# Performance work log

Measured on AMD Instinct MI355X. Metric: run time of the kernel, lower is better.

Reference implementation:

```python
import jax, jax.numpy as jnp
import numpy as np

N = 96        # num_nodes
D = 64        # emb_size / n_hid
BS = 16
T = 13
G = 1         # num_graph

# all N^2 ordered pairs, receiver-major: edge e=i*N+j has receiver i, sender j
_REC = jnp.repeat(jnp.arange(N), N)
_SEND = jnp.tile(jnp.arange(N), N)


def _lin(shape, key, scale=0.05):
    return (jax.random.normal(key, shape, dtype=jnp.float32) * scale)


def setup_inputs() -> dict:
    key = jax.random.key(0)
    ks = jax.random.split(key, 24)
    inp = {
        "skill_seq": jax.random.randint(ks[0], (BS, T), 0, N, dtype=jnp.int32),
        "adj": jax.random.uniform(ks[1], (G, BS, N, N), dtype=jnp.float32),
        "node_embeddings": jax.random.normal(ks[2], (G, N, D), dtype=jnp.float32),
        # edge MLP
        "W_msg1": _lin((2 * D, D), ks[3]), "b_msg1": jnp.zeros((D,), jnp.float32),
        "W_msg2": _lin((D, D), ks[4]),     "b_msg2": jnp.zeros((D,), jnp.float32),
        # GRU hidden projections (no bias)
        "W_hr": _lin((D, D), ks[5]), "W_hi": _lin((D, D), ks[6]), "W_hh": _lin((D, D), ks[7]),
        # GRU input projections (bias)
        "W_ir": _lin((D, D), ks[8]),  "b_ir": jnp.zeros((D,), jnp.float32),
        "W_ii": _lin((D, D), ks[9]),  "b_ii": jnp.zeros((D,), jnp.float32),
        "W_in": _lin((D, D), ks[10]), "b_in": jnp.zeros((D,), jnp.float32),
        # output MLP
        "W_o1": _lin((D, D), ks[11]), "b_o1": jnp.zeros((D,), jnp.float32),
        "W_o2": _lin((D, D), ks[12]), "b_o2": jnp.zeros((D,), jnp.float32),
        "W_o3": _lin((D, D), ks[13]), "b_o3": jnp.zeros((D,), jnp.float32),
    }
    return inp


def _forward(skill_seq, adj, node_embeddings,
             W_msg1, b_msg1, W_msg2, b_msg2,
             W_hr, W_hi, W_hh,
             W_ir, b_ir, W_ii, b_ii, W_in, b_in,
             W_o1, b_o1, W_o2, b_o2, W_o3, b_o3):
    bs, time_steps = skill_seq.shape
    hidden0 = jnp.zeros((G, bs, N, D), dtype=adj.dtype)
    emb = node_embeddings[0]  # [N, D] (num_graph=1)

    def step(hidden, skill_t):
        # gather senders/receivers over the node axis -> [G, bs, N^2, 2D]
        senders = hidden[:, :, _SEND, :]
        receivers = hidden[:, :, _REC, :]
        pre_msg = jnp.concatenate([senders, receivers], axis=-1)
        msg = jnp.tanh(pre_msg @ W_msg1 + b_msg1)        # [G, bs, N^2, D]
        msg = jnp.tanh(msg @ W_msg2 + b_msg2)
        msg = msg.reshape(G, bs, N, N, D)                # receiver i, sender j
        # mask by adjacency and scatter-sum over senders, then /N
        agg = jnp.einsum('gbij,gbijd->gbid', adj, msg) / N   # [G, bs, N, D]
        inputs = emb[skill_t][None, :, None, :]          # [1, bs, 1, D]
        r = jax.nn.sigmoid(inputs @ W_ir + b_ir + agg @ W_hr)
        i = jax.nn.sigmoid(inputs @ W_ii + b_ii + agg @ W_hi)
        n = jnp.tanh(inputs @ W_in + b_in + r * (agg @ W_hh))
        hidden = (1.0 - i) * n + i * hidden
        pred = jax.nn.relu(hidden @ W_o1 + b_o1)
        pred = jax.nn.relu(pred @ W_o2 + b_o2)
        pred = pred @ W_o3 + b_o3                        # [G, bs, N, D]
        return hidden, pred

    skills_t = skill_seq[:, :time_steps - 1].T           # [T-1, bs]
    _, preds = jax.lax.scan(step, hidden0, skills_t)     # [T-1, G, bs, N, D]
    # torch: stack(dim=1) -> [G, T-1, bs, N, D]; transpose(1,2) -> [G, bs, T-1, N, D]
    return jnp.transpose(preds, (1, 2, 0, 3, 4))


def reference(skill_seq, adj, node_embeddings,
              W_msg1, b_msg1, W_msg2, b_msg2,
              W_hr, W_hi, W_hh,
              W_ir, b_ir, W_ii, b_ii, W_in, b_in,
              W_o1, b_o1, W_o2, b_o2, W_o3, b_o3):
    return _forward(skill_seq, adj, node_embeddings,
                    W_msg1, b_msg1, W_msg2, b_msg2,
                    W_hr, W_hi, W_hh,
                    W_ir, b_ir, W_ii, b_ii, W_in, b_in,
                    W_o1, b_o1, W_o2, b_o2, W_o3, b_o3)
```

## Files before the change

### kernel.cpp

```cpp
#include <hip/hip_runtime.h>

typedef unsigned short ushort_t;
typedef __attribute__((ext_vector_type(8))) short short8;
typedef __attribute__((ext_vector_type(8))) __bf16 bf16x8;
typedef __attribute__((ext_vector_type(4))) float floatx4;

#define NN 96
#define DD 64
#define BSZ 16
#define TSTEP 12
#define JSPLIT 4
#define JPW 24
#define ITILES 6

#define OFF_HALL  0u
#define OFF_E     5111808u
#define OFF_S0    5185536u
#define OFF_S1    5578752u
#define OFF_R0    5971968u
#define OFF_R1    6365184u
#define OFF_PART  6758400u
#define OFF_WSWZ  9904128u
#define OFF_CNT   9977856u
#define HSLOT     98304

union fragU  { short8 s; bf16x8 b; };
union packU  { floatx4 f; unsigned long long u[2]; };

static __device__ __forceinline__ short f2bf(float f){
    union { float f; unsigned u; } v; v.f = f;
    unsigned u = v.u;
    u += 0x7fffu + ((u >> 16) & 1u);
    return (short)(u >> 16);
}
static __device__ __forceinline__ float fast_tanh(float x){
    float p = __expf(2.f * x);
    return (p - 1.f) * __builtin_amdgcn_rcpf(p + 1.f);
}
static __device__ __forceinline__ float fast_sigmoid(float x){
    float p = __expf(-x);
    return __builtin_amdgcn_rcpf(1.f + p);
}
static __device__ __forceinline__ void zero4(floatx4* a){
    floatx4 z = {0.f,0.f,0.f,0.f};
    a[0]=z; a[1]=z; a[2]=z; a[3]=z;
}
static __device__ __forceinline__ floatx4 aload4(const float* p){
    const unsigned long long* s = (const unsigned long long*)p;
    packU pk;
    pk.u[0] = __hip_atomic_load(s,     __ATOMIC_RELAXED, __HIP_MEMORY_SCOPE_AGENT);
    pk.u[1] = __hip_atomic_load(s + 1, __ATOMIC_RELAXED, __HIP_MEMORY_SCOPE_AGENT);
    return pk.f;
}
static __device__ __forceinline__ void astore4(float* p, floatx4 v){
    unsigned long long* d = (unsigned long long*)p;
    packU pk; pk.f = v;
    __hip_atomic_store(d,     pk.u[0], __ATOMIC_RELAXED, __HIP_MEMORY_SCOPE_AGENT);
    __hip_atomic_store(d + 1, pk.u[1], __ATOMIC_RELAXED, __HIP_MEMORY_SCOPE_AGENT);
}
static __device__ __forceinline__ void buildA(const float* sM, int col, int quad, short8& a0, short8& a1){
    floatx4 f0 = *(const floatx4*)&sM[col*68 + quad*8];
    floatx4 f1 = *(const floatx4*)&sM[col*68 + quad*8 + 4];
    floatx4 f2 = *(const floatx4*)&sM[col*68 + 32 + quad*8];
    floatx4 f3 = *(const floatx4*)&sM[col*68 + 32 + quad*8 + 4];
    fragU u0, u1;
    #pragma unroll
    for (int jj = 0; jj < 4; jj++){
        u0.b[jj]   = (__bf16)f0[jj];
        u0.b[4+jj] = (__bf16)f1[jj];
        u1.b[jj]   = (__bf16)f2[jj];
        u1.b[4+jj] = (__bf16)f3[jj];
    }
    a0 = u0.s; a1 = u1.s;
}
static __device__ __forceinline__ void mm16(short8 a0, short8 a1, const short8* wzm, int l, floatx4* acc){
    #pragma unroll
    for (int nt = 0; nt < 4; nt++){
        short8 b0 = wzm[nt*64 + l];
        short8 b1 = wzm[(4 + nt)*64 + l];
        acc[nt] = __builtin_amdgcn_mfma_f32_16x16x32_bf16(a0, b0, acc[nt], 0, 0, 0);
        acc[nt] = __builtin_amdgcn_mfma_f32_16x16x32_bf16(a1, b1, acc[nt], 0, 0, 0);
    }
}
static __device__ __forceinline__ void mm16r(short8 a0, short8 a1, const short8* f, floatx4* acc){
    #pragma unroll
    for (int nt = 0; nt < 4; nt++){
        acc[nt] = __builtin_amdgcn_mfma_f32_16x16x32_bf16(a0, f[nt],     acc[nt], 0, 0, 0);
        acc[nt] = __builtin_amdgcn_mfma_f32_16x16x32_bf16(a1, f[4 + nt], acc[nt], 0, 0, 0);
    }
}
static __device__ __forceinline__ short8 fragB(const float* W, int l, int kc, int nt, int koff){
    short8 r;
    int kbase = koff + kc*32 + ((l >> 4) << 3);
    int n = nt*16 + (l & 15);
    #pragma unroll
    for (int jj = 0; jj < 8; jj++) r[jj] = f2bf(W[(kbase + jj)*64 + n]);
    return r;
}
static __device__ __forceinline__ void mm16g(short8 a0, short8 a1, const float* W, int koff, int l, floatx4* acc){
    #pragma unroll
    for (int nt = 0; nt < 4; nt++){
        short8 b0 = fragB(W, l, 0, nt, koff);
        short8 b1 = fragB(W, l, 1, nt, koff);
        acc[nt] = __builtin_amdgcn_mfma_f32_16x16x32_bf16(a0, b0, acc[nt], 0, 0, 0);
        acc[nt] = __builtin_amdgcn_mfma_f32_16x16x32_bf16(a1, b1, acc[nt], 0, 0, 0);
    }
}

__global__ __launch_bounds__(256) void k_init(
    const float* __restrict__ emb, const float* __restrict__ Wmsg1,
    const float* __restrict__ Wmsg2,
    const float* __restrict__ Whr, const float* __restrict__ Whi, const float* __restrict__ Whh,
    const float* __restrict__ Wir, const float* __restrict__ bir,
    const float* __restrict__ Wii, const float* __restrict__ bii,
    const float* __restrict__ Win, const float* __restrict__ bin,
    const float* __restrict__ Wo1, const float* __restrict__ Wo2, const float* __restrict__ Wo3,
    const float* __restrict__ adj, const float* __restrict__ b1in, const float* __restrict__ b2in,
    const int* __restrict__ skills,
    int* __restrict__ cnt, float* __restrict__ Ef, ushort_t* __restrict__ wswz,
    float* __restrict__ hall, float* __restrict__ S1, float* __restrict__ R1)
{
    __shared__ float sM[16*68];
    __shared__ float sG[3][16*68];
    __shared__ float sE[3*64];
    __shared__ float sRS[16*17];

    int wg = blockIdx.x, tid = threadIdx.x;
    if (wg < 72) {
        int flat = wg*256 + tid;
        int m = flat / 6144; int r = flat % 6144; int s = r >> 6; int d = r & 63;
        const float* W = (m==0)? Wir : (m==1)? Wii : Win;
        const float* B = (m==0)? bir : (m==1)? bii : bin;
        float acc = B[d];
        #pragma unroll 8
        for (int k = 0; k < 64; k++)
            acc += emb[s*64 + k] * W[k*64 + d];
        Ef[flat] = acc;
        if (wg < 5) {
            int c = wg*256 + tid;
            if (c < TSTEP*BSZ*ITILES) cnt[c] = 0;
        }
        return;
    }
    if (wg < 216) {
        int flat = (wg - 72)*256 + tid;
        int m = flat >> 12; int q = flat & 4095;
        int jj = q & 7, lane = (q >> 3) & 63, nt = (q >> 9) & 3, kc = q >> 11;
        int k = kc*32 + ((lane >> 4) << 3) + jj;
        int n = nt*16 + (lane & 15);
        const float* src; int idx = k*64 + n;
        switch (m) {
          case 0: src = Wmsg2; break;
          case 1: src = Whr;  break;
          case 2: src = Whi;  break;
          case 3: src = Whh;  break;
          case 4: src = Wmsg1; break;
          case 5: src = Wmsg1; idx = (64 + k)*64 + n; break;
          case 6: src = Wo1; break;
          case 7: src = Wo2; break;
          default: src = Wo3; break;
        }
        wswz[flat] = (ushort_t)f2bf(src[idx]);
        return;
    }

    int tile = wg - 216; int b = tile / 6, it = tile % 6;
    int w = tid >> 6; int l = tid & 63;
    int quad = l >> 4, col = l & 15;

    {
        int i = tid >> 4, seg = tid & 15;
        const float* arow = &adj[(b*NN + it*16 + i)*NN + seg*6];
        float s = 0.f;
        #pragma unroll
        for (int j = 0; j < 6; j++) s += arow[j];
        sRS[i*17 + seg] = s;
    }
    if (tid < 192) {
        int m = tid >> 6, d = tid & 63;
        int s = skills[b*13 + 0];
        const float* W = (m==0)? Wir : (m==1)? Wii : Win;
        const float* B = (m==0)? bir : (m==1)? bii : bin;
        float acc = B[d];
        #pragma unroll 8
        for (int k = 0; k < 64; k++)
            acc += emb[s*64 + k] * W[k*64 + d];
        sE[tid] = acc;
    }
    __syncthreads();
    if (tid < 16) {
        float s = 0.f;
        #pragma unroll
        for (int q = 0; q < 16; q++) s += sRS[tid*17 + q];
        sRS[tid*17 + 16] = s * (1.f/96.f);
    }
    __syncthreads();

    if (w == 0) {
        float b2v[4];
        #pragma unroll
        for (int nt = 0; nt < 4; nt++) b2v[nt] = b2in[nt*16 + col];
        fragU u0, u1;
        #pragma unroll
        for (int e = 0; e < 8; e++) {
            u0.b[e] = (__bf16)fast_tanh(b1in[quad*8 + e]);
            u1.b[e] = (__bf16)fast_tanh(b1in[32 + quad*8 + e]);
        }
        floatx4 acc[4];
        zero4(acc);
        mm16g(u0.s, u1.s, Wmsg2, 0, l, acc);
        #pragma unroll
        for (int nt = 0; nt < 4; nt++)
          #pragma unroll
          for (int r = 0; r < 4; r++) {
            float m = fast_tanh(acc[nt][r] + b2v[nt]);
            sM[(quad*4 + r)*68 + nt*16 + col] = sRS[(quad*4 + r)*17 + 16] * m;
          }
    }
    __syncthreads();

    if (w < 3) {
        const float* Wg = (w==0)? Whr : (w==1)? Whi : Whh;
        short8 a0, a1;
        buildA(sM, col, quad, a0, a1);
        floatx4 acc[4];
        zero4(acc);
        mm16g(a0, a1, Wg, 0, l, acc);
        #pragma unroll
        for (int nt = 0; nt < 4; nt++)
          #pragma unroll
          for (int r = 0; r < 4; r++)
            sG[w][(quad*4 + r)*68 + nt*16 + col] = acc[nt][r];
    }
    __syncthreads();

    {
        int i = tid >> 4, k4 = (tid & 15)*4;
        float h[4];
        #pragma unroll
        for (int e = 0; e < 4; e++) {
            int d = k4 + e;
            float gi = fast_sigmoid(sE[64 + d] + sG[1][i*68 + d]);
            float gr = fast_sigmoid(sE[d]      + sG[0][i*68 + d]);
            float nv = fast_tanh  (sE[128 + d] + gr * sG[2][i*68 + d]);
            h[e] = (1.f - gi)*nv;
        }
        #pragma unroll
        for (int e = 0; e < 4; e++) sM[i*68 + k4 + e] = h[e];
        floatx4 hv = { h[0], h[1], h[2], h[3] };
        *(floatx4*)&hall[(size_t)1*HSLOT + (b*NN + it*16 + i)*64 + k4] = hv;
    }
    __syncthreads();

    if (w < 2) {
        short8 a0, a1;
        buildA(sM, col, quad, a0, a1);
        floatx4 acc[4];
        zero4(acc);
        mm16g(a0, a1, Wmsg1, w*64, l, acc);
        float* dst = (w == 0) ? S1 : R1;
        #pragma unroll
        for (int nt = 0; nt < 4; nt++)
          #pragma unroll
          for (int r = 0; r < 4; r++)
            dst[(b*NN + it*16 + quad*4 + r)*64 + nt*16 + col] = acc[nt][r];
    }
}

__global__ __launch_bounds__(512, 2) void k_step(
    const float* __restrict__ adj, const float* __restrict__ b1in, const float* __restrict__ b2in,
    const float* __restrict__ Sread, const float* __restrict__ Rread,
    const ushort_t* __restrict__ wswz, float* __restrict__ partial,
    const int* __restrict__ skills, const float* __restrict__ Ef,
    const float* __restrict__ hprev, float* __restrict__ hcur,
    float* __restrict__ Swrite, float* __restrict__ Rwrite,
    int* __restrict__ cnt, int t)
{
    __shared__ float lds[11712];
    __shared__ int sLast;
    float* sS   = lds;
    float* sRB  = lds + 1536;
    float* sAdj = lds + 2624;
    float* sAgg = lds + 3008;

    int wg = blockIdx.x;
    int js = wg / 96; int rem = wg % 96; int b = rem / 6; int it = rem % 6;
    int tid = threadIdx.x; int w = tid >> 6; int l = tid & 63;
    int quad = l >> 4, col = l & 15;
    int j0 = js * JPW;
    floatx4 myp;

    for (int q = tid; q < JPW*16; q += 512) {
        int row = q >> 4, c4 = (q & 15) * 4;
        *(floatx4*)&sS[row*64 + c4] = *(const floatx4*)&Sread[(b*NN + j0 + row)*64 + c4];
    }
    if (tid < 256) {
        int row = tid >> 4, c4 = (tid & 15) * 4;
        floatx4 r4 = *(const floatx4*)&Rread[(b*NN + it*16 + row)*64 + c4];
        floatx4 b4 = *(const floatx4*)&b1in[c4];
        floatx4 o = r4 + b4;
        *(floatx4*)&sRB[row*68 + c4] = o;
    }
    if (tid < 16*JPW) {
        int i = tid / JPW, j = tid % JPW;
        sAdj[tid] = adj[(b*NN + it*16 + i)*NN + j0 + j];
    }
    const short8* wz = (const short8*)wswz;
    short8 w2f[2][4];
    #pragma unroll
    for (int kc = 0; kc < 2; kc++)
      #pragma unroll
      for (int nt = 0; nt < 4; nt++)
        w2f[kc][nt] = wz[(kc*4 + nt)*64 + l];
    float b2v[4];
    #pragma unroll
    for (int nt = 0; nt < 4; nt++) b2v[nt] = b2in[nt*16 + col];
    __syncthreads();

    float rbv[16];
    #pragma unroll
    for (int c = 0; c < 4; c++)
        *(floatx4*)&rbv[c*4] = *(const floatx4*)&sRB[col*68 + (c>>1)*32 + quad*8 + (c&1)*4];

    float agg[4][4];
    #pragma unroll
    for (int nt=0;nt<4;nt++)
      #pragma unroll
      for (int r=0;r<4;r++) agg[nt][r] = 0.f;

    #pragma unroll
    for (int c = 0; c < 3; c++) {
        int jl = w*3 + c;
        float sv[16];
        #pragma unroll
        for (int cc = 0; cc < 4; cc++)
            *(floatx4*)&sv[cc*4] = *(const floatx4*)&sS[jl*64 + (cc>>1)*32 + quad*8 + (cc&1)*4];
        fragU u0, u1;
        #pragma unroll
        for (int e = 0; e < 8; e++) {
            u0.b[e] = (__bf16)fast_tanh(sv[e]   + rbv[e]);
            u1.b[e] = (__bf16)fast_tanh(sv[8+e] + rbv[8+e]);
        }
        floatx4 acc[4];
        zero4(acc);
        #pragma unroll
        for (int nt = 0; nt < 4; nt++) {
            acc[nt] = __builtin_amdgcn_mfma_f32_16x16x32_bf16(u0.s, w2f[0][nt], acc[nt], 0,0,0);
            acc[nt] = __builtin_amdgcn_mfma_f32_16x16x32_bf16(u1.s, w2f[1][nt], acc[nt], 0,0,0);
        }
        float adjv[4];
        #pragma unroll
        for (int r = 0; r < 4; r++) adjv[r] = sAdj[(quad*4 + r)*JPW + jl];
        #pragma unroll
        for (int nt = 0; nt < 4; nt++)
          #pragma unroll
          for (int r = 0; r < 4; r++)
            agg[nt][r] += adjv[r] * fast_tanh(acc[nt][r] + b2v[nt]);
    }
    #pragma unroll
    for (int nt = 0; nt < 4; nt++)
      #pragma unroll
      for (int r = 0; r < 4; r++)
        sAgg[w*1088 + (quad*4 + r)*68 + nt*16 + col] = agg[nt][r];
    __syncthreads();
    if (tid < 256) {
        int i = tid >> 4, k4 = (tid & 15) * 4;
        floatx4 o = {0.f,0.f,0.f,0.f};
        #pragma unroll
        for (int s8 = 0; s8 < 8; s8++)
            o += *(const floatx4*)&sAgg[s8*1088 + i*68 + k4];
        o = o * (1.f/96.f);
        myp = o;
        float* dstp = &partial[((js*BSZ + b)*NN + it*16 + i)*64 + k4];
        if (t == TSTEP - 1) *(floatx4*)dstp = o;
        else                astore4(dstp, o);
    }
    if (t == TSTEP - 1) return;

    __syncthreads();
    if (tid == 0) {
        int old = atomicAdd(&cnt[t*(BSZ*ITILES) + b*ITILES + it], 1);
        sLast = (old == JSPLIT - 1);
    }
    __syncthreads();
    if (!sLast) return;

    float* sM = lds;
    float* sG = lds + 1088;
    float* sH = lds + 4352;
    float* sE = lds + 5376;

    const short8* wzb = (const short8*)wswz;
    short8 fG[8], fSR[8];
    if (w < 3) {
        #pragma unroll
        for (int q = 0; q < 8; q++) fG[q] = wzb[(1 + w)*512 + q*64 + l];
    }
    if (w < 2) {
        #pragma unroll
        for (int q = 0; q < 8; q++) fSR[q] = wzb[(4 + w)*512 + q*64 + l];
    }

    if (tid < 256) {
        int i = tid >> 4, k4 = (tid & 15) * 4;
        floatx4 a = {0.f,0.f,0.f,0.f};
        #pragma unroll
        for (int p = 0; p < JSPLIT; p++) {
            if (p == js) a += myp;
            else         a += aload4(&partial[((p*BSZ + b)*NN + it*16 + i)*64 + k4]);
        }
        *(floatx4*)&sM[i*68 + k4] = a;
        *(floatx4*)&sH[i*64 + k4] = *(const floatx4*)&hprev[(b*NN + it*16 + i)*64 + k4];
    } else if (tid < 448) {
        int q = tid - 256;
        int s = skills[b*13 + t];
        sE[q] = Ef[(q >> 6)*6144 + s*64 + (q & 63)];
    }
    __syncthreads();

    if (w < 3) {
        short8 a0, a1;
        buildA(sM, col, quad, a0, a1);
        floatx4 acc[4];
        zero4(acc);
        mm16r(a0, a1, fG, acc);
        #pragma unroll
        for (int nt = 0; nt < 4; nt++)
          #pragma unroll
          for (int r = 0; r < 4; r++)
            sG[w*1088 + (quad*4 + r)*68 + nt*16 + col] = acc[nt][r];
    }
    __syncthreads();

    if (tid < 256) {
        int i = tid >> 4, k4 = (tid & 15) * 4;
        float h[4];
        #pragma unroll
        for (int e = 0; e < 4; e++) {
            int d = k4 + e;
            float gr = fast_sigmoid(sE[d]       + sG[0*1088 + i*68 + d]);
            float gi = fast_sigmoid(sE[64 + d]  + sG[1*1088 + i*68 + d]);
            float nv = fast_tanh  (sE[128 + d] + gr * sG[2*1088 + i*68 + d]);
            h[e] = (1.f - gi)*nv + gi*sH[i*64 + d];
        }
        #pragma unroll
        for (int e = 0; e < 4; e++) sM[i*68 + k4 + e] = h[e];
        floatx4 hv = { h[0], h[1], h[2], h[3] };
        *(floatx4*)&hcur[(b*NN + it*16 + i)*64 + k4] = hv;
    }
    __syncthreads();

    if (w < 2) {
        short8 a0, a1;
        buildA(sM, col, quad, a0, a1);
        floatx4 acc[4];
        zero4(acc);
        mm16r(a0, a1, fSR, acc);
        float* dst = (w == 0) ? Swrite : Rwrite;
        #pragma unroll
        for (int nt = 0; nt < 4; nt++)
          #pragma unroll
          for (int r = 0; r < 4; r++)
            dst[(b*NN + it*16 + quad*4 + r)*64 + nt*16 + col] = acc[nt][r];
    }
}

__global__ __launch_bounds__(256) void k_out(
    const int* __restrict__ skills, const float* __restrict__ partial,
    const float* __restrict__ Ef, const float* __restrict__ hall,
    const ushort_t* __restrict__ wswz,
    const float* __restrict__ bo1, const float* __restrict__ bo2, const float* __restrict__ bo3,
    float* __restrict__ out)
{
    __shared__ float sT[4][16*68];
    int tid = threadIdx.x; int w = tid >> 6; int l = tid & 63;
    int quad = l >> 4, col = l & 15;
    int g = blockIdx.x*4 + w;
    int ts = g / 96; int rem = g % 96; int b = rem / 6, it = rem % 6;
    float* sm = sT[w];

    if (ts < 11) {
        const float* hsrc = hall + (size_t)(ts + 1)*HSLOT + (b*NN + it*16)*64;
        int i = l >> 2, c0 = (l & 3)*16;
        #pragma unroll
        for (int cc = 0; cc < 4; cc++)
            *(floatx4*)&sm[i*68 + c0 + cc*4] = *(const floatx4*)&hsrc[i*64 + c0 + cc*4];
    } else {
        int i = l >> 2, c0 = (l & 3)*16;
        floatx4 a[4]; zero4(a);
        for (int p = 0; p < JSPLIT; p++) {
            const float* base = &partial[((p*BSZ + b)*NN + it*16 + i)*64 + c0];
            #pragma unroll
            for (int cc = 0; cc < 4; cc++) a[cc] += *(const floatx4*)&base[cc*4];
        }
        #pragma unroll
        for (int cc = 0; cc < 4; cc++) *(floatx4*)&sm[i*68 + c0 + cc*4] = a[cc];

        short8 a0, a1; buildA(sm, col, quad, a0, a1);
        floatx4 Ar[4], Ai[4], Ah[4];
        zero4(Ar); zero4(Ai); zero4(Ah);
        mm16(a0, a1, (const short8*)wswz + 1*512, l, Ar);
        mm16(a0, a1, (const short8*)wswz + 2*512, l, Ai);
        mm16(a0, a1, (const short8*)wswz + 3*512, l, Ah);
        int s = skills[b*13 + 11];
        const float* hp = hall + 11*(size_t)HSLOT;
        #pragma unroll
        for (int nt = 0; nt < 4; nt++) {
            int d = nt*16 + col;
            float er = Ef[0*6144 + s*64 + d];
            float ei = Ef[1*6144 + s*64 + d];
            float en = Ef[2*6144 + s*64 + d];
            #pragma unroll
            for (int r = 0; r < 4; r++) {
                int row = it*16 + quad*4 + r;
                float gr = fast_sigmoid(er + Ar[nt][r]);
                float gi = fast_sigmoid(ei + Ai[nt][r]);
                float nv = fast_tanh  (en + gr*Ah[nt][r]);
                sm[(quad*4 + r)*68 + d] = (1.f - gi)*nv + gi*hp[(b*NN + row)*64 + d];
            }
        }
    }

    float bv1[4], bv2[4], bv3[4];
    #pragma unroll
    for (int nt = 0; nt < 4; nt++) {
        bv1[nt] = bo1[nt*16 + col];
        bv2[nt] = bo2[nt*16 + col];
        bv3[nt] = bo3[nt*16 + col];
    }
    short8 a0, a1;
    floatx4 acc[4];

    buildA(sm, col, quad, a0, a1);
    zero4(acc);
    mm16(a0, a1, (const short8*)wswz + 6*512, l, acc);
    #pragma unroll
    for (int nt = 0; nt < 4; nt++)
      #pragma unroll
      for (int r = 0; r < 4; r++)
        sm[(quad*4 + r)*68 + nt*16 + col] = fmaxf(0.f, acc[nt][r] + bv1[nt]);

    buildA(sm, col, quad, a0, a1);
    zero4(acc);
    mm16(a0, a1, (const short8*)wswz + 7*512, l, acc);
    #pragma unroll
    for (int nt = 0; nt < 4; nt++)
      #pragma unroll
      for (int r = 0; r < 4; r++)
        sm[(quad*4 + r)*68 + nt*16 + col] = fmaxf(0.f, acc[nt][r] + bv2[nt]);

    buildA(sm, col, quad, a0, a1);
    zero4(acc);
    mm16(a0, a1, (const short8*)wswz + 8*512, l, acc);
    #pragma unroll
    for (int nt = 0; nt < 4; nt++)
      #pragma unroll
      for (int r = 0; r < 4; r++)
        out[((b*TSTEP + ts)*NN + it*16 + quad*4 + r)*64 + nt*16 + col] = acc[nt][r] + bv3[nt];
}

extern "C" void kernel_launch(void* const* d_in, const int* in_sizes, int n_in,
                              void* d_out, int out_size, void* d_ws, size_t ws_size,
                              hipStream_t stream) {
    const int*   skills = (const int*)d_in[0];
    const float* adj    = (const float*)d_in[1];
    const float* emb    = (const float*)d_in[2];
    const float* Wmsg1  = (const float*)d_in[3];
    const float* b1     = (const float*)d_in[4];
    const float* Wmsg2  = (const float*)d_in[5];
    const float* b2     = (const float*)d_in[6];
    const float* Whr    = (const float*)d_in[7];
    const float* Whi    = (const float*)d_in[8];
    const float* Whh    = (const float*)d_in[9];
    const float* Wir    = (const float*)d_in[10];
    const float* bir    = (const float*)d_in[11];
    const float* Wii    = (const float*)d_in[12];
    const float* bii    = (const float*)d_in[13];
    const float* Win    = (const float*)d_in[14];
    const float* bin    = (const float*)d_in[15];
    const float* Wo1    = (const float*)d_in[16];
    const float* bo1    = (const float*)d_in[17];
    const float* Wo2    = (const float*)d_in[18];
    const float* bo2    = (const float*)d_in[19];
    const float* Wo3    = (const float*)d_in[20];
    const float* bo3    = (const float*)d_in[21];

    char* ws = (char*)d_ws;
    float*    hall    = (float*)(ws + OFF_HALL);
    float*    Ef      = (float*)(ws + OFF_E);
    float*    S0      = (float*)(ws + OFF_S0);
    float*    S1      = (float*)(ws + OFF_S1);
    float*    R0      = (float*)(ws + OFF_R0);
    float*    R1      = (float*)(ws + OFF_R1);
    float*    partial = (float*)(ws + OFF_PART);
    ushort_t* wswz    = (ushort_t*)(ws + OFF_WSWZ);
    int*      cnt     = (int*)(ws + OFF_CNT);
    float*    out     = (float*)d_out;

    k_init<<<dim3(312), dim3(256), 0, stream>>>(emb, Wmsg1, Wmsg2, Whr, Whi, Whh,
        Wir, bir, Wii, bii, Win, bin, Wo1, Wo2, Wo3,
        adj, b1, b2, skills, cnt, Ef, wswz, hall, S1, R1);

    for (int t = 1; t < TSTEP; t++) {
        const float* Sr = (t & 1) ? S1 : S0;
        const float* Rr = (t & 1) ? R1 : R0;
        float*       Sw = (t & 1) ? S0 : S1;
        float*       Rw = (t & 1) ? R0 : R1;
        k_step<<<dim3(JSPLIT*BSZ*ITILES), dim3(512), 0, stream>>>(
            adj, b1, b2, Sr, Rr, wswz, partial, skills, Ef,
            hall + (size_t)t*HSLOT, hall + (size_t)(t+1)*HSLOT,
            Sw, Rw, cnt, t);
    }
    k_out<<<dim3(288), dim3(256), 0, stream>>>(skills, partial, Ef, hall, wswz,
        bo1, bo2, bo3, out);
}
```

Before: 253.6 us.

## Fold output MLP for earlier timesteps into idle step blocks

Moves the output MLP for timestep t-1 into k_step, where the first non-last block of each tile computes it from the previous hidden state instead of returning idle. The final k_out launch now only handles the last two timesteps, so it shrinks from 288 to 48 blocks. The intent is to hide output-MLP work inside the step kernels' idle blocks and cut the serial tail of k_out. In exchange, k_step carries more code and register pressure, and the tile whose first-arriving block does this work may finish a little later.

```diff
diff --git a/kernel.cpp b/kernel.cpp
--- a/kernel.cpp
+++ b/kernel.cpp
@@ -105,6 +105,48 @@
         acc[nt] = __builtin_amdgcn_mfma_f32_16x16x32_bf16(a0, b0, acc[nt], 0, 0, 0);
         acc[nt] = __builtin_amdgcn_mfma_f32_16x16x32_bf16(a1, b1, acc[nt], 0, 0, 0);
     }
+}
+static __device__ __forceinline__ void mlp_tile(
+    float* sm, const ushort_t* wswz,
+    const float* bo1, const float* bo2, const float* bo3,
+    float* out, int b, int ts, int it, int l, int quad, int col)
+{
+    float bv1[4], bv2[4], bv3[4];
+    #pragma unroll
+    for (int nt = 0; nt < 4; nt++) {
+        bv1[nt] = bo1[nt*16 + col];
+        bv2[nt] = bo2[nt*16 + col];
+        bv3[nt] = bo3[nt*16 + col];
+    }
+    short8 a0, a1;
+    floatx4 acc[4];
+
+    buildA(sm, col, quad, a0, a1);
+    zero4(acc);
+    mm16(a0, a1, (const short8*)wswz + 6*512, l, acc);
+    #pragma unroll
+    for (int nt = 0; nt < 4; nt++)
+      #pragma unroll
+      for (int r = 0; r < 4; r++)
+        sm[(quad*4 + r)*68 + nt*16 + col] = fmaxf(0.f, acc[nt][r] + bv1[nt]);
+
+    buildA(sm, col, quad, a0, a1);
+    zero4(acc);
+    mm16(a0, a1, (const short8*)wswz + 7*512, l, acc);
+    #pragma unroll
+    for (int nt = 0; nt < 4; nt++)
+      #pragma unroll
+      for (int r = 0; r < 4; r++)
+        sm[(quad*4 + r)*68 + nt*16 + col] = fmaxf(0.f, acc[nt][r] + bv2[nt]);
+
+    buildA(sm, col, quad, a0, a1);
+    zero4(acc);
+    mm16(a0, a1, (const short8*)wswz + 8*512, l, acc);
+    #pragma unroll
+    for (int nt = 0; nt < 4; nt++)
+      #pragma unroll
+      for (int r = 0; r < 4; r++)
+        out[((b*TSTEP + ts)*NN + it*16 + quad*4 + r)*64 + nt*16 + col] = acc[nt][r] + bv3[nt];
 }
 
 __global__ __launch_bounds__(256) void k_init(
@@ -274,10 +316,12 @@
     const int* __restrict__ skills, const float* __restrict__ Ef,
     const float* __restrict__ hprev, float* __restrict__ hcur,
     float* __restrict__ Swrite, float* __restrict__ Rwrite,
-    int* __restrict__ cnt, int t)
+    int* __restrict__ cnt,
+    const float* __restrict__ bo1, const float* __restrict__ bo2, const float* __restrict__ bo3,
+    float* __restrict__ out, int t)
 {
     __shared__ float lds[11712];
-    __shared__ int sLast;
+    __shared__ int sLast, sFirst;
     float* sS   = lds;
     float* sRB  = lds + 1536;
     float* sAdj = lds + 2624;
@@ -380,10 +424,22 @@
     __syncthreads();
     if (tid == 0) {
         int old = atomicAdd(&cnt[t*(BSZ*ITILES) + b*ITILES + it], 1);
-        sLast = (old == JSPLIT - 1);
-    }
-    __syncthreads();
-    if (!sLast) return;
+        sLast  = (old == JSPLIT - 1);
+        sFirst = (old == 0);
+    }
+    __syncthreads();
+    if (!sLast) {
+        if (sFirst && w == 0) {
+            float* sm = lds;
+            const float* hsrc = hcur - HSLOT + (b*NN + it*16)*64;
+            int i2 = l >> 2, c0 = (l & 3)*16;
+            #pragma unroll
+            for (int cc = 0; cc < 4; cc++)
+                *(floatx4*)&sm[i2*68 + c0 + cc*4] = *(const floatx4*)&hsrc[i2*64 + c0 + cc*4];
+            mlp_tile(sm, wswz, bo1, bo2, bo3, out, b, t - 1, it, l, quad, col);
+        }
+        return;
+    }
 
     float* sM = lds;
     float* sG = lds + 1088;
@@ -476,11 +532,11 @@
     int tid = threadIdx.x; int w = tid >> 6; int l = tid & 63;
     int quad = l >> 4, col = l & 15;
     int g = blockIdx.x*4 + w;
-    int ts = g / 96; int rem = g % 96; int b = rem / 6, it = rem % 6;
+    int ts = 10 + g / 96; int rem = g % 96; int b = rem / 6, it = rem % 6;
     float* sm = sT[w];
 
-    if (ts < 11) {
-        const float* hsrc = hall + (size_t)(ts + 1)*HSLOT + (b*NN + it*16)*64;
+    if (ts == 10) {
+        const float* hsrc = hall + (size_t)11*HSLOT + (b*NN + it*16)*64;
         int i = l >> 2, c0 = (l & 3)*16;
         #pragma unroll
         for (int cc = 0; cc < 4; cc++)
@@ -520,43 +576,7 @@
             }
         }
     }
-
-    float bv1[4], bv2[4], bv3[4];
-    #pragma unroll
-    for (int nt = 0; nt < 4; nt++) {
-        bv1[nt] = bo1[nt*16 + col];
-        bv2[nt] = bo2[nt*16 + col];
-        bv3[nt] = bo3[nt*16 + col];
-    }
-    short8 a0, a1;
-    floatx4 acc[4];
-
-    buildA(sm, col, quad, a0, a1);
-    zero4(acc);
-    mm16(a0, a1, (const short8*)wswz + 6*512, l, acc);
-    #pragma unroll
-    for (int nt = 0; nt < 4; nt++)
-      #pragma unroll
-      for (int r = 0; r < 4; r++)
-        sm[(quad*4 + r)*68 + nt*16 + col] = fmaxf(0.f, acc[nt][r] + bv1[nt]);
-
-    buildA(sm, col, quad, a0, a1);
-    zero4(acc);
-    mm16(a0, a1, (const short8*)wswz + 7*512, l, acc);
-    #pragma unroll
-    for (int nt = 0; nt < 4; nt++)
-      #pragma unroll
-      for (int r = 0; r < 4; r++)
-        sm[(quad*4 + r)*68 + nt*16 + col] = fmaxf(0.f, acc[nt][r] + bv2[nt]);
-
-    buildA(sm, col, quad, a0, a1);
-    zero4(acc);
-    mm16(a0, a1, (const short8*)wswz + 8*512, l, acc);
-    #pragma unroll
-    for (int nt = 0; nt < 4; nt++)
-      #pragma unroll
-      for (int r = 0; r < 4; r++)
-        out[((b*TSTEP + ts)*NN + it*16 + quad*4 + r)*64 + nt*16 + col] = acc[nt][r] + bv3[nt];
+    mlp_tile(sm, wswz, bo1, bo2, bo3, out, b, ts, it, l, quad, col);
 }
 
 extern "C" void kernel_launch(void* const* d_in, const int* in_sizes, int n_in,
@@ -609,8 +629,8 @@
         k_step<<<dim3(JSPLIT*BSZ*ITILES), dim3(512), 0, stream>>>(
             adj, b1, b2, Sr, Rr, wswz, partial, skills, Ef,
             hall + (size_t)t*HSLOT, hall + (size_t)(t+1)*HSLOT,
-            Sw, Rw, cnt, t);
-    }
-    k_out<<<dim3(288), dim3(256), 0, stream>>>(skills, partial, Ef, hall, wswz,
+            Sw, Rw, cnt, bo1, bo2, bo3, out, t);
+    }
+    k_out<<<dim3(48), dim3(256), 0, stream>>>(skills, partial, Ef, hall, wswz,
         bo1, bo2, bo3, out);
 }
```

New measurement: 252.8 us. About the same (-0.3%).
